# Performance work log

Measured on AMD Instinct MI355X. Metric: run time of the kernel, lower is better.

The kernel has to match this reference:

```python
import jax, jax.numpy as jnp
import numpy as np

EPS = 1e-6


def gaussian_filt(x, k, sigma):
    # x: [B,H,W,C]; depthwise gaussian conv with reflect padding, matching
    # TCFormer guassian_filt (kernel uses analytic 1/(2*pi*var) normalization).
    C = x.shape[-1]
    coords = jnp.arange(k, dtype=x.dtype)
    mean = (k - 1) / 2.0
    var = float(sigma) ** 2
    g1 = jnp.exp(-(coords - mean) ** 2 / (2.0 * var))
    gk = (g1[:, None] * g1[None, :]) / (2.0 * np.pi * var)  # [k,k]
    w = jnp.tile(gk[:, :, None, None], (1, 1, 1, C))  # HWIO, depthwise
    pad = (k - 1) // 2
    xp = jnp.pad(x, ((0, 0), (pad, pad), (pad, pad), (0, 0)), mode='reflect')
    return jax.lax.conv_general_dilated(
        xp, w, (1, 1), 'VALID',
        dimension_numbers=('NHWC', 'HWIO', 'NHWC'), feature_group_count=C)


def token2map(x, loc, H, W, kernel_size, sigma):
    # Scatter-mean tokens x [B,N,C] at normalized locations loc [B,N,2] in [-1,1]
    # onto an HxW grid, then gaussian-splat to fill holes. Returns NHWC map.
    B, N, C = x.shape
    loc = jnp.clip(loc, -1.0, 1.0)
    px = jnp.clip(jnp.round(0.5 * (loc[..., 0] + 1.0) * W - 0.5).astype(jnp.int32), 0, W - 1)
    py = jnp.clip(jnp.round(0.5 * (loc[..., 1] + 1.0) * H - 0.5).astype(jnp.int32), 0, H - 1)
    idx = py * W + px + jnp.arange(B, dtype=jnp.int32)[:, None] * (H * W)  # [B,N]
    src = jnp.concatenate([x, jnp.ones((B, N, 1), x.dtype)], axis=-1)  # [B,N,C+1]
    out = jnp.zeros((B * H * W, C + 1), x.dtype).at[idx.reshape(-1)].add(src.reshape(-1, C + 1))
    out = out.reshape(B, H, W, C + 1)
    feat, cnt = out[..., :C], out[..., C:]
    feat = feat / (cnt + EPS)
    mask = (cnt > 0).astype(x.dtype)
    feat = feat * mask
    if kernel_size > 1:
        # reconstruct_feature: fill empty cells with gaussian-interpolated values
        y = gaussian_filt(jnp.concatenate([feat, mask], axis=-1), kernel_size, sigma)
        fi, mi = y[..., :C], y[..., C:]
        fi = fi / (mi + EPS)
        fi = fi * (mi > 0).astype(x.dtype)
        feat = feat + (1.0 - mask) * fi
    return feat  # [B,H,W,C]


def layernorm(x, g, b, eps=1e-5):
    m = jnp.mean(x, axis=-1, keepdims=True)
    v = jnp.var(x, axis=-1, keepdims=True)
    return (x - m) / jnp.sqrt(v + eps) * g + b


def setup_inputs() -> dict:
    key = jax.random.key(0)
    ks = jax.random.split(key, 8)
    B, N, C, H, W = 8, 16384, 64, 128, 128
    SR = 8
    std = 0.02
    return {
        'x': jax.random.normal(ks[0], (B, N, C), jnp.float32),
        'x_source': jax.random.normal(ks[1], (B, N, C), jnp.float32),
        'loc_source': jax.random.uniform(ks[2], (B, N, 2), jnp.float32) * 2.0 - 1.0,
        'conf_source': jax.random.normal(ks[3], (B, N, 1), jnp.float32) * 0.1,
        'q_w': jax.random.normal(ks[4], (C, C), jnp.float32) * std,
        'kv_w': jax.random.normal(ks[5], (2 * C, C), jnp.float32) * std,
        'sr_w': jax.random.normal(ks[6], (SR, SR, C, C), jnp.float32) * np.sqrt(2.0 / (SR * SR * C)),
        'sr_b': jnp.zeros((C,), jnp.float32),
        'norm_w': jnp.ones((C,), jnp.float32),
        'norm_b': jnp.zeros((C,), jnp.float32),
        'proj_w': jax.random.normal(ks[7], (C, C), jnp.float32) * std,
        'proj_b': jnp.zeros((C,), jnp.float32),
        'H': H,
        'W': W,
    }


def reference(x, x_source, loc_source, conf_source, q_w, kv_w, sr_w, sr_b,
              norm_w, norm_b, proj_w, proj_b, H, W):
    B, N, C = x.shape
    num_heads = 1  # PVT stage-1
    hd = C // num_heads
    scale = hd ** -0.5
    sr = sr_w.shape[0]  # sr_ratio = 8

    # q projection: [B, nh, N, hd]
    q = (x @ q_w.T).reshape(B, N, num_heads, hd).transpose(0, 2, 1, 3)

    # token2map scatter-splat (kernel = sr_ratio + 1, sigma = 2)
    feat = token2map(x_source, loc_source, H, W, sr + 1, 2.0)  # [B,H,W,C]

    # SR conv (k = stride = sr_ratio), then layernorm
    xs = jax.lax.conv_general_dilated(
        feat, sr_w, (sr, sr), 'VALID',
        dimension_numbers=('NHWC', 'HWIO', 'NHWC')) + sr_b
    h, w = H // sr, W // sr
    xs = layernorm(xs.reshape(B, h * w, C), norm_w, norm_b)  # [B,M,C]

    # confidence map on the reduced grid (kernel_size=1 => pure scatter-mean)
    conf = token2map(conf_source, loc_source, h, w, 1, 1.0).reshape(B, h * w)  # [B,M]

    kv = (xs @ kv_w.T).reshape(B, h * w, 2, num_heads, hd)
    k = kv[:, :, 0].transpose(0, 2, 1, 3)  # [B,nh,M,hd]
    v = kv[:, :, 1].transpose(0, 2, 1, 3)

    attn = jnp.einsum('bhnd,bhmd->bhnm', q, k) * scale
    attn = attn + conf[:, None, None, :]  # additive confidence bias
    attn = jax.nn.softmax(attn, axis=-1)
    out = jnp.einsum('bhnm,bhmd->bhnd', attn, v)
    out = out.transpose(0, 2, 1, 3).reshape(B, N, C)
    return out @ proj_w.T + proj_b
```

## Files before the change

kernel.cpp:

```cpp
#include <hip/hip_runtime.h>
#include <hip/hip_bf16.h>

#define NN 16384
#define NC 64
#define GH 128
#define GW 128
#define GM 256

typedef __attribute__((ext_vector_type(8))) short bf16x8;
typedef __attribute__((ext_vector_type(4))) float f32x4;

static __device__ __forceinline__ int reflect128(int i){
  if (i < 0) i = -i;
  if (i > 127) i = 254 - i;
  return i;
}

static __device__ __forceinline__ ushort f2bf(float f){
  union { float f; unsigned u; } v; v.f = f;
  unsigned r = v.u + 0x7fffu + ((v.u >> 16) & 1u);
  return (ushort)(r >> 16);
}

static __device__ __forceinline__ int cell_of(float l, float S2, int hi){
  l = fminf(fmaxf(l, -1.f), 1.f);
  float u = l + 1.f;
  int p = (int)rintf(u*S2 - 0.5f);
  return min(max(p,0),hi);
}

__global__ __launch_bounds__(256) void k_zero(float4* __restrict__ p, int n4){
  int i = blockIdx.x*256 + threadIdx.x;
  int stride = gridDim.x*256;
  float4 z = make_float4(0.f,0.f,0.f,0.f);
  for (; i < n4; i += stride) p[i] = z;
}

__global__ __launch_bounds__(256) void k_scatter_feat(
    const float* __restrict__ xsrc, const float* __restrict__ loc,
    float* __restrict__ featg){
  int gid = blockIdx.x*256 + threadIdx.x;
  int t = gid >> 6;
  int b = t >> 14;
  int px = cell_of(loc[2*t],   64.f, 127);
  int py = cell_of(loc[2*t+1], 64.f, 127);
  int cell = (b*GH + py)*GW + px;
  atomicAdd(&featg[cell*NC + (gid & 63)], xsrc[gid]);
}

__global__ __launch_bounds__(256) void k_scatter_aux(
    const float* __restrict__ loc, const float* __restrict__ csrc,
    float* __restrict__ cnt, float* __restrict__ csum, float* __restrict__ ccnt){
  int t = blockIdx.x*256 + threadIdx.x;
  int b = t >> 14;
  int px = cell_of(loc[2*t],   64.f, 127);
  int py = cell_of(loc[2*t+1], 64.f, 127);
  atomicAdd(&cnt[(b*GH+py)*GW+px], 1.0f);
  int qx = cell_of(loc[2*t],   8.f, 15);
  int qy = cell_of(loc[2*t+1], 8.f, 15);
  int cell = b*GM + qy*16 + qx;
  atomicAdd(&csum[cell], csrc[t]);
  atomicAdd(&ccnt[cell], 1.0f);
}

__global__ __launch_bounds__(256) void k_finalize_feat(
    float* __restrict__ featg, const float* __restrict__ cnt){
  int gid = blockIdx.x*256 + threadIdx.x;
  float cn = cnt[gid>>6];
  float v  = featg[gid];
  featg[gid] = (cn > 0.f) ? v/(cn+1e-6f) : 0.f;
}

__global__ __launch_bounds__(256) void k_finalize_conf(
    const float* __restrict__ csum, const float* __restrict__ ccnt,
    float* __restrict__ conf){
  int i = blockIdx.x*256 + threadIdx.x;
  float cn = ccnt[i];
  conf[i] = (cn > 0.f) ? csum[i]/(cn+1e-6f) : 0.f;
}

__global__ __launch_bounds__(256) void k_fill2(
    const float* __restrict__ cnt, float* __restrict__ feat){
  int gid = blockIdx.x*256 + threadIdx.x;
  int p = gid >> 2, cg = gid & 3;
  if (cnt[p] > 0.f) return;
  int b = p>>14, py=(p>>7)&127, px=p&127;
  const float fn = 0.039788735772973836f;
  float g1[9];
  #pragma unroll
  for (int i=0;i<9;++i){ float d=(float)i-4.f; g1[i]=__expf(-d*d*0.125f); }
  float4 acc[4];
  #pragma unroll
  for (int i=0;i<4;++i) acc[i]=make_float4(0.f,0.f,0.f,0.f);
  float msum=0.f;
  for (int dy=0; dy<9; ++dy){
    int iy = reflect128(py-4+dy);
    for (int dx=0; dx<9; ++dx){
      int ix = reflect128(px-4+dx);
      int q  = (b*GH+iy)*GW+ix;
      if (cnt[q] <= 0.f) continue;
      float wn = g1[dy]*g1[dx]*fn;
      msum += wn;
      const float4* fr = (const float4*)&feat[q*NC + cg*16];
      #pragma unroll
      for (int k=0;k<4;++k){
        float4 vv = fr[k];
        acc[k].x += wn*vv.x; acc[k].y += wn*vv.y;
        acc[k].z += wn*vv.z; acc[k].w += wn*vv.w;
      }
    }
  }
  if (msum <= 0.f) return;
  float inv = 1.f/(msum + 1e-6f);
  float4* o = (float4*)&feat[p*NC + cg*16];
  #pragma unroll
  for (int k=0;k<4;++k)
    o[k] = make_float4(acc[k].x*inv, acc[k].y*inv, acc[k].z*inv, acc[k].w*inv);
}

static __device__ __forceinline__ int rowswz(int bid){
  return ((bid & 7) << 7) + (bid >> 3);
}

__global__ __launch_bounds__(256) void k_finfillh(
    float* __restrict__ feat, const float* __restrict__ cnt,
    float* __restrict__ feath, float* __restrict__ maskh){
  __shared__ float F[GW*NC];
  __shared__ float CR[GW];
  int py = rowswz(blockIdx.x), t = threadIdx.x;
  const float fn = 0.039788735772973836f;
  float g1n[9];
  #pragma unroll
  for (int i=0;i<9;++i){ float d=(float)i-4.f; g1n[i]=__expf(-d*d*0.125f)*fn; }
  if (t < GW) CR[t] = cnt[py*GW + t];
  __syncthreads();
  for (int i=t*4; i<GW*NC; i+=1024){
    int px = i>>6;
    float cn = CR[px];
    float inv = (cn > 0.f) ? 1.f/(cn+1e-6f) : 0.f;
    float4 v = *(const float4*)&feat[(size_t)py*GW*NC + i];
    v.x*=inv; v.y*=inv; v.z*=inv; v.w*=inv;
    *(float4*)&F[i] = v;
    *(float4*)&feat[(size_t)py*GW*NC + i] = v;
  }
  __syncthreads();
  for (int i=t*4; i<GW*NC; i+=1024){
    int px = i>>6, c = i&63;
    float4 acc = make_float4(0.f,0.f,0.f,0.f);
    #pragma unroll
    for (int dx=0; dx<9; ++dx){
      int ix = reflect128(px-4+dx);
      float w = g1n[dx];
      float4 v = *(const float4*)&F[ix*NC + c];
      acc.x += w*v.x; acc.y += w*v.y; acc.z += w*v.z; acc.w += w*v.w;
    }
    *(float4*)&feath[(size_t)py*GW*NC + i] = acc;
  }
  if (t < GW){
    float hm = 0.f;
    #pragma unroll
    for (int dx=0; dx<9; ++dx){
      int ix = reflect128(t-4+dx);
      hm += g1n[dx]*((CR[ix] > 0.f) ? 1.f : 0.f);
    }
    maskh[py*GW + t] = hm;
  }
}

__global__ __launch_bounds__(256) void k_fillv(
    float* __restrict__ feat, const float* __restrict__ cnt,
    const float* __restrict__ feath, const float* __restrict__ maskh){
  int pyg = rowswz(blockIdx.x), t = threadIdx.x;
  int b = pyg >> 7, pyl = pyg & 127;
  int px = t>>1, c0 = (t&1)<<5;
  float g1[9];
  #pragma unroll
  for (int i=0;i<9;++i){ float d=(float)i-4.f; g1[i]=__expf(-d*d*0.125f); }
  float cn = cnt[pyg*GW + px];
  float ym = 0.f;
  int ry[9];
  #pragma unroll
  for (int dy=0; dy<9; ++dy){
    ry[dy] = b*GH + reflect128(pyl-4+dy);
    ym += g1[dy]*maskh[ry[dy]*GW + px];
  }
  if (cn > 0.f || ym <= 0.f) return;
  float inv = 1.f/(ym + 1e-6f);
  float4 acc[8];
  #pragma unroll
  for (int k=0;k<8;++k) acc[k]=make_float4(0.f,0.f,0.f,0.f);
  #pragma unroll
  for (int dy=0; dy<9; ++dy){
    float w = g1[dy];
    const float4* hf = (const float4*)&feath[((size_t)ry[dy]*GW+px)*NC + c0];
    #pragma unroll
    for (int k=0;k<8;++k){
      float4 v = hf[k];
      acc[k].x += w*v.x; acc[k].y += w*v.y; acc[k].z += w*v.z; acc[k].w += w*v.w;
    }
  }
  float4* o = (float4*)&feat[((size_t)pyg*GW+px)*NC + c0];
  #pragma unroll
  for (int k=0;k<8;++k)
    o[k] = make_float4(acc[k].x*inv, acc[k].y*inv, acc[k].z*inv, acc[k].w*inv);
}

__global__ __launch_bounds__(256) void k_srconv(
    const float* __restrict__ feat, const float* __restrict__ srw,
    float* __restrict__ xs0){
  alignas(16) __shared__ float A[64*65];
  alignas(16) __shared__ float Bs[64*64];
  int mt = blockIdx.x, kh = blockIdx.y;
  int t = threadIdx.x;
  int tm = t>>4, tn = t&15;
  float acc[4][4] = {{0.f}};
  for (int kc=0; kc<8; ++kc){
    __syncthreads();
    for (int idx=t; idx<4096; idx+=256){
      int mr = idx>>6, kk = idx&63;
      int m = mt*64+mr;
      int b = m>>8, oh=(m>>4)&15, ow=m&15;
      A[mr*65+kk] = feat[(((b*GH)+(oh*8+kh))*GW + ow*8)*NC + kc*64 + kk];
    }
    for (int idx=t; idx<4096; idx+=256)
      Bs[idx] = srw[(kh*512 + kc*64)*64 + idx];
    __syncthreads();
    for (int kk=0; kk<64; ++kk){
      float4 bv = *(const float4*)&Bs[kk*64 + tn*4];
      #pragma unroll
      for (int i=0;i<4;++i){
        float av = A[(tm*4+i)*65 + kk];
        acc[i][0] += av*bv.x; acc[i][1] += av*bv.y;
        acc[i][2] += av*bv.z; acc[i][3] += av*bv.w;
      }
    }
  }
  #pragma unroll
  for (int i=0;i<4;++i)
    #pragma unroll
    for (int j=0;j<4;++j)
      atomicAdd(&xs0[(mt*64+tm*4+i)*64 + tn*4+j], acc[i][j]);
}

__global__ __launch_bounds__(256) void k_srconv2(
    const float* __restrict__ feat, const float* __restrict__ srw,
    float* __restrict__ part){
  alignas(16) __shared__ float A[64*65];
  alignas(16) __shared__ float Bs[64*64];
  int mt = blockIdx.x, kh = blockIdx.y, kq = blockIdx.z;
  int t = threadIdx.x;
  int tm = t>>4, tn = t&15;
  float acc[4][4] = {{0.f}};
  for (int kc=0; kc<4; ++kc){
    int kw = kq*4 + kc;
    __syncthreads();
    for (int idx=t; idx<4096; idx+=256){
      int mr = idx>>6, kk = idx&63;
      int m = mt*64+mr;
      int b = m>>8, oh=(m>>4)&15, ow=m&15;
      A[mr*65+kk] = feat[(((b*GH)+(oh*8+kh))*GW + ow*8 + kw)*NC + kk];
    }
    for (int idx=t; idx<4096; idx+=256)
      Bs[idx] = srw[(kh*512 + kw*64)*64 + idx];
    __syncthreads();
    for (int kk=0; kk<64; ++kk){
      float4 bv = *(const float4*)&Bs[kk*64 + tn*4];
      #pragma unroll
      for (int i=0;i<4;++i){
        float av = A[(tm*4+i)*65 + kk];
        acc[i][0] += av*bv.x; acc[i][1] += av*bv.y;
        acc[i][2] += av*bv.z; acc[i][3] += av*bv.w;
      }
    }
  }
  float* pdst = part + (size_t)(kh*2+kq)*2048*64;
  #pragma unroll
  for (int i=0;i<4;++i)
    #pragma unroll
    for (int j=0;j<4;++j)
      pdst[(mt*64+tm*4+i)*64 + tn*4+j] = acc[i][j];
}

__global__ __launch_bounds__(256) void k_ln(
    const float* __restrict__ xs0, const float* __restrict__ srb,
    const float* __restrict__ nw, const float* __restrict__ nbv,
    float* __restrict__ xs){
  int row  = blockIdx.x*4 + (threadIdx.x>>6);
  int lane = threadIdx.x & 63;
  float v = xs0[row*64+lane] + srb[lane];
  float s = v;
  #pragma unroll
  for (int off=32; off; off>>=1) s += __shfl_xor(s, off, 64);
  float mean = s*(1.f/64.f);
  float d = v - mean;
  float s2 = d*d;
  #pragma unroll
  for (int off=32; off; off>>=1) s2 += __shfl_xor(s2, off, 64);
  float var = s2*(1.f/64.f);
  xs[row*64+lane] = d*(1.f/sqrtf(var+1e-5f))*nw[lane] + nbv[lane];
}

__global__ __launch_bounds__(256) void k_kv1(
    const float* __restrict__ xs, const float* __restrict__ kvw,
    float* __restrict__ kraw, float* __restrict__ vraw){
  int gid = blockIdx.x*256 + threadIdx.x;
  int r = gid >> 6, d = gid & 63;
  const float* xr = &xs[r*64];
  float ka=0.f, va=0.f;
  for (int c=0;c<64;++c){
    float xc = xr[c];
    ka += xc*kvw[d*64+c];
    va += xc*kvw[(64+d)*64+c];
  }
  kraw[gid] = ka;
  vraw[gid] = va;
}

__global__ __launch_bounds__(256) void k_kvproj2(
    const float* __restrict__ kraw, const float* __restrict__ vraw,
    const float* __restrict__ qw, const float* __restrict__ pw,
    ushort* __restrict__ KB, ushort* __restrict__ VB){
  int gid = blockIdx.x*256 + threadIdx.x;
  int r = gid >> 6, c = gid & 63;
  int b = r >> 8, m = r & 255;
  const float* kr = &kraw[r*64];
  const float* vr = &vraw[r*64];
  float ak=0.f, av=0.f;
  for (int i=0;i<64;++i){
    ak += kr[i]*qw[i*64+c];
    av += vr[i]*pw[c*64+i];
  }
  {
    int nt = m>>4, l15 = m&15, kb = c>>5, h = (c>>3)&3, j = c&7;
    KB[((((b*16 + nt)*2 + kb)*4 + h)*16 + l15)*8 + j] = f2bf(ak);
  }
  {
    int ct = c>>4, n15 = c&15, kb2 = m>>5, h2 = (m>>3)&3, j2 = m&7;
    VB[((((b*4 + ct)*8 + kb2)*4 + h2)*16 + n15)*8 + j2] = f2bf(av);
  }
}

__global__ __launch_bounds__(256) void k_kvfused(
    const float* __restrict__ part, const float* __restrict__ srb,
    const float* __restrict__ nw, const float* __restrict__ nbv,
    const float* __restrict__ kvw, const float* __restrict__ qw,
    const float* __restrict__ pw,
    ushort* __restrict__ KB, ushort* __restrict__ VB){
  __shared__ float XR[4][64], KR[4][64], VR[4][64];
  int t = threadIdx.x;
  int rl = t>>6, d = t&63;
  int r  = blockIdx.x*4 + rl;
  float v = srb[d];
  #pragma unroll
  for (int ps=0; ps<16; ++ps)
    v += part[(size_t)ps*2048*64 + r*64 + d];
  float s = v;
  #pragma unroll
  for (int off=32; off; off>>=1) s += __shfl_xor(s, off, 64);
  float mean = s*(1.f/64.f);
  float dd = v - mean;
  float s2 = dd*dd;
  #pragma unroll
  for (int off=32; off; off>>=1) s2 += __shfl_xor(s2, off, 64);
  float var = s2*(1.f/64.f);
  XR[rl][d] = dd*(1.f/sqrtf(var+1e-5f))*nw[d] + nbv[d];
  __syncthreads();
  float ka=0.f, va=0.f;
  for (int cc=0; cc<64; ++cc){
    float xc = XR[rl][cc];
    ka += xc*kvw[d*64+cc];
    va += xc*kvw[(64+d)*64+cc];
  }
  KR[rl][d] = ka; VR[rl][d] = va;
  __syncthreads();
  int c = d;
  float ak=0.f, av=0.f;
  for (int i=0;i<64;++i){
    ak += KR[rl][i]*qw[i*64+c];
    av += VR[rl][i]*pw[c*64+i];
  }
  int b = r>>8, m = r&255;
  {
    int nt = m>>4, l15 = m&15, kb = c>>5, h = (c>>3)&3, j = c&7;
    KB[((((b*16 + nt)*2 + kb)*4 + h)*16 + l15)*8 + j] = f2bf(ak);
  }
  {
    int ct = c>>4, n15 = c&15, kb2 = m>>5, h2 = (m>>3)&3, j2 = m&7;
    VB[((((b*4 + ct)*8 + kb2)*4 + h2)*16 + n15)*8 + j2] = f2bf(av);
  }
}

__global__ __launch_bounds__(256) void k_attn5(
    const float* __restrict__ x, const ushort* __restrict__ KB,
    const ushort* __restrict__ VB, const float* __restrict__ conf,
    const float* __restrict__ projb, float* __restrict__ out){
  alignas(16) __shared__ ushort P[4*4096];
  int t = threadIdx.x, w = t>>6, l = t&63;
  int b = blockIdx.x >> 8;
  int row0 = ((blockIdx.x & 255) << 6) + (w<<4);
  int l15 = l & 15, h = l >> 4;
  const ushort* KBb = KB + b*16384;
  const ushort* VBb = VB + b*16384;
  bf16x8 xa[2];
  {
    const float* xr = x + (size_t)(b*NN + row0 + l15)*64 + h*8;
    #pragma unroll
    for (int kb=0; kb<2; ++kb){
      float4 a0 = *(const float4*)(xr + 32*kb);
      float4 a1 = *(const float4*)(xr + 32*kb + 4);
      bf16x8 v;
      v[0]=(short)f2bf(a0.x); v[1]=(short)f2bf(a0.y);
      v[2]=(short)f2bf(a0.z); v[3]=(short)f2bf(a0.w);
      v[4]=(short)f2bf(a1.x); v[5]=(short)f2bf(a1.y);
      v[6]=(short)f2bf(a1.z); v[7]=(short)f2bf(a1.w);
      xa[kb]=v;
    }
  }
  f32x4 acc[16];
  #pragma unroll
  for (int nt=0;nt<16;++nt) acc[nt] = (f32x4){0.f,0.f,0.f,0.f};
  #pragma unroll
  for (int nt=0;nt<16;++nt){
    bf16x8 b0 = *(const bf16x8*)(KBb + (nt*2+0)*512 + l*8);
    bf16x8 b1 = *(const bf16x8*)(KBb + (nt*2+1)*512 + l*8);
    acc[nt] = __builtin_amdgcn_mfma_f32_16x16x32_bf16(xa[0], b0, acc[nt], 0,0,0);
    acc[nt] = __builtin_amdgcn_mfma_f32_16x16x32_bf16(xa[1], b1, acc[nt], 0,0,0);
  }
  float rs[4] = {0.f,0.f,0.f,0.f};
  ushort* Pw = P + w*4096;
  #pragma unroll
  for (int nt=0;nt<16;++nt){
    float cf = conf[b*GM + nt*16 + l15];
    #pragma unroll
    for (int reg=0;reg<4;++reg){
      float p = __expf(fmaf(acc[nt][reg], 0.125f, cf));
      rs[reg] += p;
      int m   = nt*16 + l15;
      int row = h*4 + reg;
      int ld  = ((m>>3)&3)*16 + row;
      int idx = ((m>>5)*512 + ld*8 + (m&7)) ^ (ld & 0x38);
      Pw[idx] = f2bf(p);
    }
  }
  #pragma unroll
  for (int off=1; off<16; off<<=1){
    #pragma unroll
    for (int reg=0;reg<4;++reg) rs[reg] += __shfl_xor(rs[reg], off, 64);
  }
  f32x4 oacc[4];
  #pragma unroll
  for (int ct=0;ct<4;++ct) oacc[ct] = (f32x4){0.f,0.f,0.f,0.f};
  #pragma unroll
  for (int kb2=0;kb2<8;++kb2){
    int ridx = (kb2*512 + l*8) ^ (l & 0x38);
    bf16x8 pa = *(const bf16x8*)(Pw + ridx);
    #pragma unroll
    for (int ct=0;ct<4;++ct){
      bf16x8 vb = *(const bf16x8*)(VBb + (ct*8+kb2)*512 + l*8);
      oacc[ct] = __builtin_amdgcn_mfma_f32_16x16x32_bf16(pa, vb, oacc[ct], 0,0,0);
    }
  }
  float* OT = (float*)Pw;
  #pragma unroll
  for (int ct=0;ct<4;++ct){
    float pb4 = projb[ct*16 + l15];
    #pragma unroll
    for (int reg=0;reg<4;++reg)
      OT[(h*4+reg)*68 + ct*16 + l15] = oacc[ct][reg]/rs[reg] + pb4;
  }
  #pragma unroll
  for (int i=0;i<4;++i){
    int row = i*4 + h;
    float4 v = *(const float4*)&OT[row*68 + l15*4];
    *(float4*)&out[(size_t)(b*NN + row0 + row)*64 + l15*4] = v;
  }
}

__global__ __launch_bounds__(256) void k_attn6(
    const float* __restrict__ x, const ushort* __restrict__ KB,
    const ushort* __restrict__ VB, const float* __restrict__ conf,
    const float* __restrict__ projb, float* __restrict__ out){
  alignas(16) __shared__ ushort P[4*4096];
  int t = threadIdx.x, w = t>>6, l = t&63;
  int b = blockIdx.x >> 8;
  int row0 = ((blockIdx.x & 255) << 6) + (w<<4);
  int l15 = l & 15, h = l >> 4;
  const ushort* KBb = KB + b*16384;
  const ushort* VBb = VB + b*16384;

  bf16x8 xa[2];
  {
    const float* xr = x + (size_t)(b*NN + row0 + l15)*64 + h*8;
    #pragma unroll
    for (int kb=0; kb<2; ++kb){
      float4 a0 = *(const float4*)(xr + 32*kb);
      float4 a1 = *(const float4*)(xr + 32*kb + 4);
      bf16x8 v;
      v[0]=(short)f2bf(a0.x); v[1]=(short)f2bf(a0.y);
      v[2]=(short)f2bf(a0.z); v[3]=(short)f2bf(a0.w);
      v[4]=(short)f2bf(a1.x); v[5]=(short)f2bf(a1.y);
      v[6]=(short)f2bf(a1.z); v[7]=(short)f2bf(a1.w);
      xa[kb]=v;
    }
  }

  float rs[4] = {0.f,0.f,0.f,0.f};
  f32x4 oacc[4];
  #pragma unroll
  for (int ct=0;ct<4;++ct) oacc[ct] = (f32x4){0.f,0.f,0.f,0.f};
  ushort* Pw = P + w*4096;

  #pragma unroll
  for (int c=0;c<4;++c){
    f32x4 acc[4];
    #pragma unroll
    for (int q=0;q<4;++q) acc[q] = (f32x4){0.f,0.f,0.f,0.f};
    #pragma unroll
    for (int q=0;q<4;++q){
      int nt = c*4 + q;
      bf16x8 b0 = *(const bf16x8*)(KBb + (nt*2+0)*512 + l*8);
      bf16x8 b1 = *(const bf16x8*)(KBb + (nt*2+1)*512 + l*8);
      acc[q] = __builtin_amdgcn_mfma_f32_16x16x32_bf16(xa[0], b0, acc[q], 0,0,0);
      acc[q] = __builtin_amdgcn_mfma_f32_16x16x32_bf16(xa[1], b1, acc[q], 0,0,0);
    }
    #pragma unroll
    for (int q=0;q<4;++q){
      int nt = c*4 + q;
      float cf = conf[b*GM + nt*16 + l15];
      #pragma unroll
      for (int reg=0;reg<4;++reg){
        float p = __expf(fmaf(acc[q][reg], 0.125f, cf));
        rs[reg] += p;
        int m   = nt*16 + l15;
        int row = h*4 + reg;
        int ld  = ((m>>3)&3)*16 + row;
        int idx = ((m>>5)*512 + ld*8 + (m&7)) ^ (ld & 0x38);
        Pw[idx] = f2bf(p);
      }
    }
    #pragma unroll
    for (int kk=0;kk<2;++kk){
      int kb2 = c*2 + kk;
      int ridx = (kb2*512 + l*8) ^ (l & 0x38);
      bf16x8 pa = *(const bf16x8*)(Pw + ridx);
      #pragma unroll
      for (int ct=0;ct<4;++ct){
        bf16x8 vb = *(const bf16x8*)(VBb + (ct*8+kb2)*512 + l*8);
        oacc[ct] = __builtin_amdgcn_mfma_f32_16x16x32_bf16(pa, vb, oacc[ct], 0,0,0);
      }
    }
  }

  #pragma unroll
  for (int off=1; off<16; off<<=1){
    #pragma unroll
    for (int reg=0;reg<4;++reg) rs[reg] += __shfl_xor(rs[reg], off, 64);
  }

  float* OT = (float*)Pw;
  #pragma unroll
  for (int ct=0;ct<4;++ct){
    float pb4 = projb[ct*16 + l15];
    #pragma unroll
    for (int reg=0;reg<4;++reg)
      OT[(h*4+reg)*68 + ct*16 + l15] = oacc[ct][reg]/rs[reg] + pb4;
  }
  #pragma unroll
  for (int i=0;i<4;++i){
    int row = i*4 + h;
    float4 v = *(const float4*)&OT[row*68 + l15*4];
    *(float4*)&out[(size_t)(b*NN + row0 + row)*64 + l15*4] = v;
  }
}

extern "C" void kernel_launch(void* const* d_in, const int* in_sizes, int n_in,
                              void* d_out, int out_size, void* d_ws, size_t ws_size,
                              hipStream_t stream){
  const float* x    = (const float*)d_in[0];
  const float* xsrc = (const float*)d_in[1];
  const float* loc  = (const float*)d_in[2];
  const float* csrc = (const float*)d_in[3];
  const float* qw   = (const float*)d_in[4];
  const float* kvw  = (const float*)d_in[5];
  const float* srw  = (const float*)d_in[6];
  const float* srb  = (const float*)d_in[7];
  const float* nw   = (const float*)d_in[8];
  const float* nbv  = (const float*)d_in[9];
  const float* pw   = (const float*)d_in[10];
  const float* pb   = (const float*)d_in[11];
  float* out = (float*)d_out;
  float* ws = (float*)d_ws;

  size_t of_feat  = 0;
  size_t of_cnt   = of_feat  + 8ull*GH*GW*NC;
  size_t of_csum  = of_cnt   + 8ull*GH*GW;
  size_t of_ccnt  = of_csum  + 8ull*GM;
  size_t zero_end = of_ccnt  + 8ull*GM;
  size_t of_feath = zero_end;
  size_t of_maskh = of_feath + 8ull*GH*GW*NC;
  size_t of_part  = of_maskh + 8ull*GH*GW;
  size_t of_conf  = of_part  + 16ull*2048*64;
  size_t of_kb    = of_conf  + 8ull*GM;
  size_t of_vb    = of_kb    + 8ull*8192;
  size_t total_p  = of_vb    + 8ull*8192;

  if (ws_size >= total_p*sizeof(float)){
    k_zero         <<<2048,        256, 0, stream>>>((float4*)ws, (int)(zero_end>>2));
    k_scatter_feat <<<8*NN*NC/256, 256, 0, stream>>>(xsrc, loc, ws+of_feat);
    k_scatter_aux  <<<8*NN/256,    256, 0, stream>>>(loc, csrc, ws+of_cnt, ws+of_csum, ws+of_ccnt);
    k_finalize_conf<<<8*GM/256,    256, 0, stream>>>(ws+of_csum, ws+of_ccnt, ws+of_conf);
    k_finfillh     <<<8*GH,        256, 0, stream>>>(ws+of_feat, ws+of_cnt, ws+of_feath, ws+of_maskh);
    k_fillv        <<<8*GH,        256, 0, stream>>>(ws+of_feat, ws+of_cnt, ws+of_feath, ws+of_maskh);
    dim3 gconv(32, 8, 2);
    k_srconv2      <<<gconv,       256, 0, stream>>>(ws+of_feat, srw, ws+of_part);
    k_kvfused      <<<8*GM/4,      256, 0, stream>>>(ws+of_part, srb, nw, nbv, kvw, qw, pw,
                                                     (ushort*)(ws+of_kb), (ushort*)(ws+of_vb));
    k_attn6        <<<8*NN/64,     256, 0, stream>>>(x, (const ushort*)(ws+of_kb),
                                                     (const ushort*)(ws+of_vb),
                                                     ws+of_conf, pb, out);
  } else {
    size_t f_feat = 0;
    size_t f_cnt  = f_feat + 8ull*GH*GW*NC;
    size_t f_csum = f_cnt  + 8ull*GH*GW;
    size_t f_ccnt = f_csum + 8ull*GM;
    size_t f_xs0  = f_ccnt + 8ull*GM;
    size_t f_zero = f_xs0  + 8ull*GM*NC;
    size_t f_conf = f_zero;
    size_t f_xs   = f_conf + 8ull*GM;
    size_t f_kr   = f_xs   + 8ull*GM*NC;
    size_t f_vr   = f_kr   + 8ull*GM*NC;
    size_t f_kb   = f_vr   + 8ull*GM*NC;
    size_t f_vb   = f_kb   + 8ull*8192;
    hipMemsetAsync(ws, 0, f_zero*sizeof(float), stream);
    k_scatter_feat <<<8*NN*NC/256, 256, 0, stream>>>(xsrc, loc, ws+f_feat);
    k_scatter_aux  <<<8*NN/256,    256, 0, stream>>>(loc, csrc, ws+f_cnt, ws+f_csum, ws+f_ccnt);
    k_finalize_feat<<<8*GH*GW*NC/256, 256, 0, stream>>>(ws+f_feat, ws+f_cnt);
    k_finalize_conf<<<8*GM/256,    256, 0, stream>>>(ws+f_csum, ws+f_ccnt, ws+f_conf);
    k_fill2        <<<8*GH*GW*4/256, 256, 0, stream>>>(ws+f_cnt, ws+f_feat);
    dim3 gconv(8*GM/64, 8);
    k_srconv       <<<gconv,       256, 0, stream>>>(ws+f_feat, srw, ws+f_xs0);
    k_ln           <<<8*GM/4,      256, 0, stream>>>(ws+f_xs0, srb, nw, nbv, ws+f_xs);
    k_kv1          <<<8*GM*NC/256, 256, 0, stream>>>(ws+f_xs, kvw, ws+f_kr, ws+f_vr);
    k_kvproj2      <<<8*GM*NC/256, 256, 0, stream>>>(ws+f_kr, ws+f_vr, qw, pw,
                                                     (ushort*)(ws+f_kb), (ushort*)(ws+f_vb));
    k_attn5        <<<8*NN/64,     256, 0, stream>>>(x, (const ushort*)(ws+f_kb),
                                                     (const ushort*)(ws+f_vb),
                                                     ws+f_conf, pb, out);
  }
}
```

Baseline: 186.9 us.

## Transpose attention MFMA operands so each lane owns a query row

The attention kernel swaps the A/B operands of both MFMA products, so the accumulator layout gives each lane four consecutive key or channel values for a single query row. As a result, softmax row sums need only two cross-lane shuffles instead of a 16-lane reduction per register. P is written to LDS as packed 8-byte stores with a new XOR swizzle, and the output is written directly with float4 stores instead of going through an LDS transpose. Confidence and projection bias are read as float4. The risk is new LDS bank-conflict patterns and correctness of the new swizzle and operand mapping.

```diff
diff --git a/kernel.cpp b/kernel.cpp
--- a/kernel.cpp
+++ b/kernel.cpp
@@ -476,7 +476,7 @@
   }
 }
 
-__global__ __launch_bounds__(256) void k_attn6(
+__global__ __launch_bounds__(256) void k_attn7(
     const float* __restrict__ x, const ushort* __restrict__ KB,
     const ushort* __restrict__ VB, const float* __restrict__ conf,
     const float* __restrict__ projb, float* __restrict__ out){
@@ -504,11 +504,12 @@
     }
   }
 
-  float rs[4] = {0.f,0.f,0.f,0.f};
+  float rs = 0.f;
   f32x4 oacc[4];
   #pragma unroll
   for (int ct=0;ct<4;++ct) oacc[ct] = (f32x4){0.f,0.f,0.f,0.f};
-  ushort* Pw = P + w*4096;
+  char* Pw = (char*)(P + w*4096);
+  int swz = (l15 & 7) << 4;
 
   #pragma unroll
   for (int c=0;c<4;++c){
@@ -518,58 +519,52 @@
     #pragma unroll
     for (int q=0;q<4;++q){
       int nt = c*4 + q;
-      bf16x8 b0 = *(const bf16x8*)(KBb + (nt*2+0)*512 + l*8);
-      bf16x8 b1 = *(const bf16x8*)(KBb + (nt*2+1)*512 + l*8);
-      acc[q] = __builtin_amdgcn_mfma_f32_16x16x32_bf16(xa[0], b0, acc[q], 0,0,0);
-      acc[q] = __builtin_amdgcn_mfma_f32_16x16x32_bf16(xa[1], b1, acc[q], 0,0,0);
+      bf16x8 k0 = *(const bf16x8*)(KBb + (nt*2+0)*512 + l*8);
+      bf16x8 k1 = *(const bf16x8*)(KBb + (nt*2+1)*512 + l*8);
+      acc[q] = __builtin_amdgcn_mfma_f32_16x16x32_bf16(k0, xa[0], acc[q], 0,0,0);
+      acc[q] = __builtin_amdgcn_mfma_f32_16x16x32_bf16(k1, xa[1], acc[q], 0,0,0);
     }
     #pragma unroll
     for (int q=0;q<4;++q){
       int nt = c*4 + q;
-      float cf = conf[b*GM + nt*16 + l15];
-      #pragma unroll
-      for (int reg=0;reg<4;++reg){
-        float p = __expf(fmaf(acc[q][reg], 0.125f, cf));
-        rs[reg] += p;
-        int m   = nt*16 + l15;
-        int row = h*4 + reg;
-        int ld  = ((m>>3)&3)*16 + row;
-        int idx = ((m>>5)*512 + ld*8 + (m&7)) ^ (ld & 0x38);
-        Pw[idx] = f2bf(p);
-      }
+      float4 cf4 = *(const float4*)&conf[b*GM + nt*16 + 4*h];
+      float p0 = __expf(fmaf(acc[q][0], 0.125f, cf4.x));
+      float p1 = __expf(fmaf(acc[q][1], 0.125f, cf4.y));
+      float p2 = __expf(fmaf(acc[q][2], 0.125f, cf4.z));
+      float p3 = __expf(fmaf(acc[q][3], 0.125f, cf4.w));
+      rs += (p0+p1) + (p2+p3);
+      uint u0 = (uint)f2bf(p0) | ((uint)f2bf(p1) << 16);
+      uint u1 = (uint)f2bf(p2) | ((uint)f2bf(p3) << 16);
+      int off = (l15*512 + nt*32 + 8*h) ^ swz;
+      *(uint2*)(Pw + off) = make_uint2(u0, u1);
     }
     #pragma unroll
     for (int kk=0;kk<2;++kk){
       int kb2 = c*2 + kk;
-      int ridx = (kb2*512 + l*8) ^ (l & 0x38);
-      bf16x8 pa = *(const bf16x8*)(Pw + ridx);
+      int roff = (l15*512 + kb2*64 + 16*h) ^ swz;
+      bf16x8 pb = *(const bf16x8*)(Pw + roff);
       #pragma unroll
       for (int ct=0;ct<4;++ct){
-        bf16x8 vb = *(const bf16x8*)(VBb + (ct*8+kb2)*512 + l*8);
-        oacc[ct] = __builtin_amdgcn_mfma_f32_16x16x32_bf16(pa, vb, oacc[ct], 0,0,0);
+        bf16x8 va = *(const bf16x8*)(VBb + (ct*8+kb2)*512 + l*8);
+        oacc[ct] = __builtin_amdgcn_mfma_f32_16x16x32_bf16(va, pb, oacc[ct], 0,0,0);
       }
     }
   }
 
-  #pragma unroll
-  for (int off=1; off<16; off<<=1){
-    #pragma unroll
-    for (int reg=0;reg<4;++reg) rs[reg] += __shfl_xor(rs[reg], off, 64);
-  }
-
-  float* OT = (float*)Pw;
+  rs += __shfl_xor(rs, 16, 64);
+  rs += __shfl_xor(rs, 32, 64);
+  float inv = 1.f/rs;
+
+  float* orow = out + (size_t)(b*NN + row0 + l15)*64 + 4*h;
   #pragma unroll
   for (int ct=0;ct<4;++ct){
-    float pb4 = projb[ct*16 + l15];
-    #pragma unroll
-    for (int reg=0;reg<4;++reg)
-      OT[(h*4+reg)*68 + ct*16 + l15] = oacc[ct][reg]/rs[reg] + pb4;
-  }
-  #pragma unroll
-  for (int i=0;i<4;++i){
-    int row = i*4 + h;
-    float4 v = *(const float4*)&OT[row*68 + l15*4];
-    *(float4*)&out[(size_t)(b*NN + row0 + row)*64 + l15*4] = v;
+    float4 pb4 = *(const float4*)&projb[ct*16 + 4*h];
+    float4 o4;
+    o4.x = fmaf(oacc[ct][0], inv, pb4.x);
+    o4.y = fmaf(oacc[ct][1], inv, pb4.y);
+    o4.z = fmaf(oacc[ct][2], inv, pb4.z);
+    o4.w = fmaf(oacc[ct][3], inv, pb4.w);
+    *(float4*)(orow + ct*16) = o4;
   }
 }
 
@@ -615,7 +610,7 @@
     k_srconv2      <<<gconv,       256, 0, stream>>>(ws+of_feat, srw, ws+of_part);
     k_kvfused      <<<8*GM/4,      256, 0, stream>>>(ws+of_part, srb, nw, nbv, kvw, qw, pw,
                                                      (ushort*)(ws+of_kb), (ushort*)(ws+of_vb));
-    k_attn6        <<<8*NN/64,     256, 0, stream>>>(x, (const ushort*)(ws+of_kb),
+    k_attn7        <<<8*NN/64,     256, 0, stream>>>(x, (const ushort*)(ws+of_kb),
                                                      (const ushort*)(ws+of_vb),
                                                      ws+of_conf, pb, out);
   } else {
```

New measurement: 198.7 us. 1.06x slower.
